# Kernel tuning notes

Measured on AMD Instinct MI355X. Metric: run time of the kernel, lower is better.

## Reference

```python
import jax, jax.numpy as jnp
import numpy as np

EMBED_DIM = 1024
NUM_HEADS = 16
HEAD_DIM = EMBED_DIM // NUM_HEADS
RANK = 512
B, S = 4, 4096


def setup_inputs() -> dict:
    key = jax.random.key(0)
    ks = jax.random.split(key, 16)
    sd = 0.02
    inp = {
        "query": jax.random.normal(ks[0], (B, S, EMBED_DIM), jnp.float32),
        "key": jax.random.normal(ks[1], (B, S, EMBED_DIM), jnp.float32),
        "value": jax.random.normal(ks[2], (B, S, EMBED_DIM), jnp.float32),
        # torch nn.Linear weights: [out_features, in_features]
        "q_down_w": jax.random.normal(ks[3], (RANK, EMBED_DIM), jnp.float32) * sd,
        "q_up_w": jax.random.normal(ks[4], (EMBED_DIM, RANK), jnp.float32) * sd,
        "q_up_b": jax.random.normal(ks[5], (EMBED_DIM,), jnp.float32) * sd,
        "k_down_w": jax.random.normal(ks[6], (RANK, EMBED_DIM), jnp.float32) * sd,
        "k_up_w": jax.random.normal(ks[7], (EMBED_DIM, RANK), jnp.float32) * sd,
        "k_up_b": jax.random.normal(ks[8], (EMBED_DIM,), jnp.float32) * sd,
        "v_down_w": jax.random.normal(ks[9], (RANK, EMBED_DIM), jnp.float32) * sd,
        "v_up_w": jax.random.normal(ks[10], (EMBED_DIM, RANK), jnp.float32) * sd,
        "v_up_b": jax.random.normal(ks[11], (EMBED_DIM,), jnp.float32) * sd,
        "out_w": jax.random.normal(ks[12], (EMBED_DIM, EMBED_DIM), jnp.float32) * sd,
        "out_b": jax.random.normal(ks[13], (EMBED_DIM,), jnp.float32) * sd,
    }
    return inp


def _linear(x, w, b=None):
    y = x @ w.T
    return y if b is None else y + b


def reference(query, key, value,
              q_down_w, q_up_w, q_up_b,
              k_down_w, k_up_w, k_up_b,
              v_down_w, v_up_w, v_up_b,
              out_w, out_b):
    b, s, _ = query.shape
    # low-rank QKV projections
    q = _linear(_linear(query, q_down_w), q_up_w, q_up_b)
    k = _linear(_linear(key, k_down_w), k_up_w, k_up_b)
    v = _linear(_linear(value, v_down_w), v_up_w, v_up_b)
    # [B,S,E] -> [B,H,S,Dh]
    q = q.reshape(b, s, NUM_HEADS, HEAD_DIM).transpose(0, 2, 1, 3)
    k = k.reshape(b, s, NUM_HEADS, HEAD_DIM).transpose(0, 2, 1, 3)
    v = v.reshape(b, s, NUM_HEADS, HEAD_DIM).transpose(0, 2, 1, 3)
    # kernel feature map: elu + 1  (note: scaling_factor in original is computed but unused)
    q = jax.nn.elu(q) + 1.0
    k = jax.nn.elu(k) + 1.0
    k_sum = k.sum(axis=-2)                              # [B,H,Dh]
    denom = jnp.einsum('bhnd,bhd->bhn', q, k_sum)       # [B,H,S]
    kv = jnp.einsum('bhnd,bhne->bhde', k, v)            # [B,H,Dh,Dh]
    num = jnp.einsum('bhnd,bhde->bhne', q, kv)          # [B,H,S,Dh]
    out = num / (denom[..., None] + 1e-6)
    out = out.transpose(0, 2, 1, 3).reshape(b, s, EMBED_DIM)
    return _linear(out, out_w, out_b)
```

## Files before the change

### kernel.cpp

```cpp
#include <hip/hip_runtime.h>
#include <hip/hip_bf16.h>

typedef unsigned short ushort_t;
typedef unsigned int uint_t;
typedef __attribute__((ext_vector_type(8))) short short8;
typedef __attribute__((ext_vector_type(4))) float f32x4;
typedef __attribute__((ext_vector_type(2))) float f32x2;

#define EMBED 1024
#define RANK  512
#define BB    4
#define SS    4096
#define HH    16
#define DHD   64
#define MM    (BB*SS)
#define NCHUNK 16

__device__ __forceinline__ float bf2f(ushort_t u) {
    union { uint_t i; float f; } v; v.i = ((uint_t)u) << 16; return v.f;
}
__device__ __forceinline__ float asf(uint_t u) {
    union { uint_t i; float f; } v; v.i = u; return v.f;
}
__device__ __forceinline__ ushort_t f2bf(float f) {
    union { float f; uint_t i; } v; v.f = f;
    uint_t r = v.i + 0x7FFFu + ((v.i >> 16) & 1u);
    return (ushort_t)(r >> 16);
}
__device__ __forceinline__ void gl2lds16(const void* g, void* l) {
    __builtin_amdgcn_global_load_lds((const __attribute__((address_space(1))) void*)g,
                                     (__attribute__((address_space(3))) void*)l,
                                     16, 0, 0);
}

template<int EPI>
__global__ __launch_bounds__(256) void gemm_bt(
    const ushort_t* __restrict__ A0, const ushort_t* __restrict__ A1, const ushort_t* __restrict__ A2,
    const ushort_t* __restrict__ B0, const ushort_t* __restrict__ B1, const ushort_t* __restrict__ B2,
    const float* __restrict__ bias0, const float* __restrict__ bias1, const float* __restrict__ bias2,
    void* __restrict__ C0, void* __restrict__ C1, void* __restrict__ C2,
    int N, int K, int nbx)
{
    __shared__ __align__(16) char lds_raw[49152];

    const int z = blockIdx.z;
    const ushort_t* Ab   = (z == 0) ? A0 : (z == 1) ? A1 : A2;
    const ushort_t* Bm   = (z == 0) ? B0 : (z == 1) ? B1 : B2;
    const float*    bias = (z == 0) ? bias0 : (z == 1) ? bias1 : bias2;
    void*           Cv   = (z == 0) ? C0 : (z == 1) ? C1 : C2;

    const int cpx = gridDim.x >> 3;
    const int bid = blockIdx.x;
    const int wg  = (bid & 7) * cpx + (bid >> 3);
    const long m0 = (long)(wg / nbx) * 128;
    const long n0 = (long)(wg % nbx) * 128;

    const int t = threadIdx.x;
    const int lane = t & 63;
    const int w = t >> 6;
    const int wr = (w >> 1) * 64;
    const int wc = (w & 1) * 64;
    const int fr = lane & 15;
    const int kq = (lane >> 4) * 8;

    const int srow = t >> 2;
    const int scol = ((t & 3) ^ ((srow >> 1) & 3)) * 8;
    const int kqs = (((kq >> 3) ^ ((fr >> 1) & 3))) * 8;

    auto STAGE = [&](int k0, int buf) {
        char* Ad = lds_raw + buf * 8192;
        char* Bd = lds_raw + 24576 + buf * 8192;
        #pragma unroll
        for (int ro = 0; ro < 2; ++ro) {
            const int row = ro * 64 + srow;
            gl2lds16(Ab + (m0 + row) * (long)K + k0 + scol, Ad + (ro * 256 + w * 64) * 16);
            gl2lds16(Bm + (n0 + row) * (long)K + k0 + scol, Bd + (ro * 256 + w * 64) * 16);
        }
    };

    f32x4 acc[4][4] = {};
    const int nt = K >> 5;

    STAGE(0, 0);
    STAGE(32, 1);

    int cur = 0;
    for (int ti = 0; ti < nt; ++ti) {
        if (ti + 1 < nt) { asm volatile("s_waitcnt vmcnt(4)" ::: "memory"); }
        else             { asm volatile("s_waitcnt vmcnt(0)" ::: "memory"); }
        __builtin_amdgcn_sched_barrier(0);
        __builtin_amdgcn_s_barrier();
        __builtin_amdgcn_sched_barrier(0);

        int nb = cur + 2; if (nb >= 3) nb -= 3;
        if (ti + 2 < nt) STAGE((ti + 2) << 5, nb);

        const ushort_t* Asc = (const ushort_t*)(lds_raw + cur * 8192);
        const ushort_t* Bsc = (const ushort_t*)(lds_raw + 24576 + cur * 8192);
        short8 av[4], bv[4];
        #pragma unroll
        for (int mi = 0; mi < 4; ++mi)
            av[mi] = *(const short8*)&Asc[(wr + mi * 16 + fr) * 32 + kqs];
        #pragma unroll
        for (int nf = 0; nf < 4; ++nf)
            bv[nf] = *(const short8*)&Bsc[(wc + nf * 16 + fr) * 32 + kqs];
        #pragma unroll
        for (int mi = 0; mi < 4; ++mi)
            #pragma unroll
            for (int nf = 0; nf < 4; ++nf)
                acc[mi][nf] = __builtin_amdgcn_mfma_f32_16x16x32_bf16(
                    av[mi], bv[nf], acc[mi][nf], 0, 0, 0);

        ++cur; if (cur == 3) cur = 0;
    }

    const int rj = (lane >> 4) * 4;
    if (EPI == 3) {
        float* Cf = (float*)Cv;
        __syncthreads();
        #pragma unroll
        for (int nf = 0; nf < 4; ++nf) {
            const long col = n0 + wc + nf * 16 + fr;
            const float bval = bias[col];
            #pragma unroll
            for (int mi = 0; mi < 4; ++mi)
                #pragma unroll
                for (int j = 0; j < 4; ++j)
                    Cf[(m0 + wr + mi * 16 + rj + j) * (long)N + col] = acc[mi][nf][j] + bval;
        }
    } else {
        ushort_t* Ct = (ushort_t*)lds_raw;
        __syncthreads();
        const bool do_elu = (EPI == 2) && (z < 2);
        #pragma unroll
        for (int nf = 0; nf < 4; ++nf) {
            const int coll = wc + nf * 16 + fr;
            const float bval = (EPI >= 2) ? bias[n0 + coll] : 0.0f;
            #pragma unroll
            for (int mi = 0; mi < 4; ++mi) {
                #pragma unroll
                for (int j = 0; j < 4; ++j) {
                    float x = acc[mi][nf][j];
                    if (EPI >= 2) x += bval;
                    if (do_elu) x = (x > 0.0f) ? (x + 1.0f) : __expf(x);
                    Ct[(wr + mi * 16 + rj + j) * 136 + coll] = f2bf(x);
                }
            }
        }
        __syncthreads();
        ushort_t* Cb = (ushort_t*)Cv;
        #pragma unroll
        for (int it = 0; it < 8; ++it) {
            const int idx = it * 256 + t;
            const int r   = idx >> 4;
            const int c8  = (idx & 15) * 8;
            short8 vv = *(const short8*)&Ct[r * 136 + c8];
            *(short8*)(Cb + (m0 + r) * (long)N + n0 + c8) = vv;
        }
    }
}

__global__ __launch_bounds__(256) void cvt_act(const float* __restrict__ q,
                                               const float* __restrict__ k,
                                               const float* __restrict__ v,
                                               ushort_t* __restrict__ qo,
                                               ushort_t* __restrict__ ko,
                                               ushort_t* __restrict__ vo)
{
    const long NTOT   = (long)3 * MM * EMBED;
    const long stride = (long)2048 * 256 * 8;
    long i = ((long)blockIdx.x * 256 + threadIdx.x) * 8;
    for (; i < NTOT; i += stride) {
        const int  zz  = (int)(i >> 24);
        const long off = i & 0xFFFFFF;
        const float* src = (zz == 0) ? q : (zz == 1) ? k : v;
        ushort_t*    dst = (zz == 0) ? qo : (zz == 1) ? ko : vo;
        f32x4 f0 = *(const f32x4*)(src + off);
        f32x4 f1 = *(const f32x4*)(src + off + 4);
        short8 h;
        h[0] = (short)f2bf(f0[0]); h[1] = (short)f2bf(f0[1]);
        h[2] = (short)f2bf(f0[2]); h[3] = (short)f2bf(f0[3]);
        h[4] = (short)f2bf(f1[0]); h[5] = (short)f2bf(f1[1]);
        h[6] = (short)f2bf(f1[2]); h[7] = (short)f2bf(f1[3]);
        *(short8*)(dst + off) = h;
    }
}

__global__ __launch_bounds__(256) void cvt_weights(
    const float* __restrict__ s0, const float* __restrict__ s1,
    const float* __restrict__ s2, const float* __restrict__ s3,
    const float* __restrict__ s4, const float* __restrict__ s5,
    const float* __restrict__ s6,
    ushort_t* __restrict__ d0, ushort_t* __restrict__ d1,
    ushort_t* __restrict__ d2, ushort_t* __restrict__ d3,
    ushort_t* __restrict__ d4, ushort_t* __restrict__ d5,
    ushort_t* __restrict__ d6)
{
    const int y = blockIdx.y;
    const float* src; ushort_t* dst; int n;
    switch (y) {
        case 0: src = s0; dst = d0; n = RANK * EMBED; break;
        case 1: src = s1; dst = d1; n = RANK * EMBED; break;
        case 2: src = s2; dst = d2; n = RANK * EMBED; break;
        case 3: src = s3; dst = d3; n = RANK * EMBED; break;
        case 4: src = s4; dst = d4; n = RANK * EMBED; break;
        case 5: src = s5; dst = d5; n = RANK * EMBED; break;
        default: src = s6; dst = d6; n = EMBED * EMBED; break;
    }
    const int i = (blockIdx.x * 256 + threadIdx.x) * 4;
    if (i < n) {
        f32x4 f = *(const f32x4*)(src + i);
        typedef __attribute__((ext_vector_type(4))) short short4v;
        short4v h;
        h[0] = (short)f2bf(f[0]); h[1] = (short)f2bf(f[1]);
        h[2] = (short)f2bf(f[2]); h[3] = (short)f2bf(f[3]);
        *(short4v*)(dst + i) = h;
    }
}

__global__ __launch_bounds__(256) void kv_stats(const ushort_t* __restrict__ Kp,
                                                const ushort_t* __restrict__ Vp,
                                                float* __restrict__ kvp,
                                                float* __restrict__ ksump)
{
    __shared__ __align__(16) ushort_t Ks[64 * 64];
    __shared__ __align__(16) ushort_t Vs[64 * 64];
    const int t = threadIdx.x;
    const int w = t >> 6;
    const int bh = blockIdx.x;
    const int chunk = blockIdx.y;
    const int b = bh >> 4, h = bh & 15;
    const int d0 = (t & 15) * 4;
    const int e0 = (t >> 4) * 4;
    f32x2 acc2[4][2] = {};
    f32x2 sks2[2] = {};
    const long hbase = ((long)b * SS) * EMBED + h * DHD;

    for (int sub = 0; sub < 4; ++sub) {
        const int n00 = chunk * 256 + sub * 64;
        #pragma unroll
        for (int ro = 0; ro < 2; ++ro) {
            const int idx = ro * 256 + t;
            const int r = idx >> 3, c16 = idx & 7;
            const long g = hbase + (long)(n00 + r) * EMBED + c16 * 8;
            gl2lds16(Kp + g, (char*)Ks + (ro * 256 + w * 64) * 16);
            gl2lds16(Vp + g, (char*)Vs + (ro * 256 + w * 64) * 16);
        }
        __syncthreads();
        #pragma unroll 8
        for (int n = 0; n < 64; ++n) {
            const uint_t* kr = (const uint_t*)(Ks + n * 64 + d0);
            const uint_t* vr = (const uint_t*)(Vs + n * 64 + e0);
            const uint_t k01 = kr[0], k23 = kr[1];
            const uint_t v01 = vr[0], v23 = vr[1];
            f32x2 kd0, kd1;
            kd0[0] = asf(k01 << 16); kd0[1] = asf(k01 & 0xffff0000u);
            kd1[0] = asf(k23 << 16); kd1[1] = asf(k23 & 0xffff0000u);
            float ve[4];
            ve[0] = asf(v01 << 16); ve[1] = asf(v01 & 0xffff0000u);
            ve[2] = asf(v23 << 16); ve[3] = asf(v23 & 0xffff0000u);
            #pragma unroll
            for (int e = 0; e < 4; ++e) {
                f32x2 vb; vb[0] = ve[e]; vb[1] = ve[e];
                acc2[e][0] += vb * kd0;
                acc2[e][1] += vb * kd1;
            }
            if (e0 == 0) { sks2[0] += kd0; sks2[1] += kd1; }
        }
        __syncthreads();
    }

    float* dst = kvp + ((long)chunk * 64 + bh) * 4096;
    #pragma unroll
    for (int e = 0; e < 4; ++e) {
        f32x4 vv;
        vv[0] = acc2[e][0][0]; vv[1] = acc2[e][0][1];
        vv[2] = acc2[e][1][0]; vv[3] = acc2[e][1][1];
        *(f32x4*)(dst + (e0 + e) * 64 + d0) = vv;
    }
    if (e0 == 0) {
        float* sd = ksump + ((long)chunk * 64 + bh) * 64 + d0;
        sd[0] = sks2[0][0]; sd[1] = sks2[0][1];
        sd[2] = sks2[1][0]; sd[3] = sks2[1][1];
    }
}

__global__ __launch_bounds__(256) void kv_reduce(const float* __restrict__ kvp,
                                                 const float* __restrict__ ksump,
                                                 ushort_t* __restrict__ kvb,
                                                 float* __restrict__ ksumf)
{
    const int bh = blockIdx.x;
    const int t = threadIdx.x;
    const long base = (long)bh * 4096 + t * 16;
    f32x4 s[4] = {};
    #pragma unroll 4
    for (int c = 0; c < NCHUNK; ++c) {
        const float* src = kvp + (long)c * 64 * 4096 + base;
        #pragma unroll
        for (int j = 0; j < 4; ++j) s[j] += *(const f32x4*)(src + j * 4);
    }
    short8 o0, o1;
    #pragma unroll
    for (int j = 0; j < 4; ++j) {
        o0[j]     = (short)f2bf(s[0][j]); o0[4 + j] = (short)f2bf(s[1][j]);
        o1[j]     = (short)f2bf(s[2][j]); o1[4 + j] = (short)f2bf(s[3][j]);
    }
    *(short8*)(kvb + base)     = o0;
    *(short8*)(kvb + base + 8) = o1;

    if (t < 64) {
        float ss = 0.f;
        #pragma unroll
        for (int c = 0; c < NCHUNK; ++c) ss += ksump[(long)c * 64 * 64 + bh * 64 + t];
        ksumf[bh * 64 + t] = ss;
    }
}

__global__ __launch_bounds__(256) void attn_out(const ushort_t* __restrict__ Qp,
                                                const ushort_t* __restrict__ kvb,
                                                const float* __restrict__ ksum,
                                                ushort_t* __restrict__ Op)
{
    __shared__ __align__(16) ushort_t Qs[128 * 64];
    __shared__ __align__(16) ushort_t KVs[64 * 64];
    __shared__ float kss[64];
    __shared__ float dnm[128];
    const int t = threadIdx.x;
    const int w = t >> 6, lane = t & 63;
    const int bh = blockIdx.x, mc = blockIdx.y;
    const int b = bh >> 4, h = bh & 15;
    const long base = ((long)b * SS + mc * 128) * EMBED + h * DHD;

    #pragma unroll
    for (int ro = 0; ro < 4; ++ro) {
        const int idx = ro * 256 + t;
        const int r = idx >> 3, c16 = idx & 7;
        gl2lds16(Qp + base + (long)r * EMBED + c16 * 8,
                 (char*)Qs + (ro * 256 + w * 64) * 16);
    }
    #pragma unroll
    for (int ro = 0; ro < 2; ++ro) {
        const int idx = ro * 256 + t;
        gl2lds16(kvb + (long)bh * 4096 + idx * 8,
                 (char*)KVs + (ro * 256 + w * 64) * 16);
    }
    if (t < 64) kss[t] = ksum[bh * 64 + t];
    __syncthreads();

    if (t < 128) {
        float s = 0.f;
        const uint_t* qr = (const uint_t*)(Qs + t * 64);
        #pragma unroll
        for (int jj = 0; jj < 32; ++jj) {
            const uint_t u = qr[jj];
            union { uint_t i; float f; } lo, hi;
            lo.i = u << 16; hi.i = u & 0xffff0000u;
            s += lo.f * kss[2 * jj] + hi.f * kss[2 * jj + 1];
        }
        dnm[t] = s;
    }

    const int fr = lane & 15, kq = (lane >> 4) * 8;
    f32x4 acc[2][4] = {};
    #pragma unroll
    for (int ks = 0; ks < 2; ++ks) {
        short8 av[2], bv[4];
        #pragma unroll
        for (int mi = 0; mi < 2; ++mi)
            av[mi] = *(const short8*)&Qs[(w * 32 + mi * 16 + fr) * 64 + ks * 32 + kq];
        #pragma unroll
        for (int nf = 0; nf < 4; ++nf)
            bv[nf] = *(const short8*)&KVs[(nf * 16 + fr) * 64 + ks * 32 + kq];
        #pragma unroll
        for (int mi = 0; mi < 2; ++mi)
            #pragma unroll
            for (int nf = 0; nf < 4; ++nf)
                acc[mi][nf] = __builtin_amdgcn_mfma_f32_16x16x32_bf16(
                    av[mi], bv[nf], acc[mi][nf], 0, 0, 0);
    }
    __syncthreads();

    const int rj = (lane >> 4) * 4;
    #pragma unroll
    for (int mi = 0; mi < 2; ++mi) {
        #pragma unroll
        for (int nf = 0; nf < 4; ++nf) {
            #pragma unroll
            for (int j = 0; j < 4; ++j) {
                const int r = w * 32 + mi * 16 + rj + j;
                const int c = nf * 16 + fr;
                const float x = acc[mi][nf][j] / (dnm[r] + 1e-6f);
                Op[base + (long)r * EMBED + c] = f2bf(x);
            }
        }
    }
}

extern "C" void kernel_launch(void* const* d_in, const int* in_sizes, int n_in,
                              void* d_out, int out_size, void* d_ws, size_t ws_size,
                              hipStream_t stream)
{
    (void)in_sizes; (void)n_in; (void)out_size; (void)ws_size;
    const float* query = (const float*)d_in[0];
    const float* key_  = (const float*)d_in[1];
    const float* value = (const float*)d_in[2];
    const float* q_dw  = (const float*)d_in[3];
    const float* q_uw  = (const float*)d_in[4];
    const float* q_ub  = (const float*)d_in[5];
    const float* k_dw  = (const float*)d_in[6];
    const float* k_uw  = (const float*)d_in[7];
    const float* k_ub  = (const float*)d_in[8];
    const float* v_dw  = (const float*)d_in[9];
    const float* v_uw  = (const float*)d_in[10];
    const float* v_ub  = (const float*)d_in[11];
    const float* o_w   = (const float*)d_in[12];
    const float* o_b   = (const float*)d_in[13];

    char* ws = (char*)d_ws;
    size_t off = 0;
    auto alloc = [&](size_t bytes) -> void* {
        void* p = ws + off;
        off += (bytes + 255) & ~(size_t)255;
        return p;
    };
    const size_t WSMALL = (size_t)RANK * EMBED;
    ushort_t* bw_qd = (ushort_t*)alloc(WSMALL * 2);
    ushort_t* bw_qu = (ushort_t*)alloc(WSMALL * 2);
    ushort_t* bw_kd = (ushort_t*)alloc(WSMALL * 2);
    ushort_t* bw_ku = (ushort_t*)alloc(WSMALL * 2);
    ushort_t* bw_vd = (ushort_t*)alloc(WSMALL * 2);
    ushort_t* bw_vu = (ushort_t*)alloc(WSMALL * 2);
    ushort_t* bw_o  = (ushort_t*)alloc((size_t)EMBED * EMBED * 2);
    ushort_t* Qb    = (ushort_t*)alloc((size_t)MM * EMBED * 2);
    ushort_t* Kb    = (ushort_t*)alloc((size_t)MM * EMBED * 2);
    ushort_t* Vb    = (ushort_t*)alloc((size_t)MM * EMBED * 2);
    ushort_t* Y1q   = (ushort_t*)alloc((size_t)MM * RANK * 2);
    ushort_t* Y1k   = (ushort_t*)alloc((size_t)MM * RANK * 2);
    ushort_t* Y1v   = (ushort_t*)alloc((size_t)MM * RANK * 2);
    float*    ksump = (float*)alloc((size_t)NCHUNK * 64 * 64 * 4);
    float*    ksumf = (float*)alloc((size_t)64 * 64 * 4);
    ushort_t* kvb   = (ushort_t*)alloc((size_t)64 * 64 * 64 * 2);

    ushort_t* PQ = Qb;
    ushort_t* PK = Kb;
    ushort_t* PV = Vb;
    float*    kvp = (float*)Y1q;
    ushort_t* O   = Y1k;

    const dim3 blk(256);

    cvt_act<<<dim3(2048), blk, 0, stream>>>(query, key_, value, Qb, Kb, Vb);
    cvt_weights<<<dim3(EMBED * EMBED / 1024, 7), blk, 0, stream>>>(
        q_dw, q_uw, k_dw, k_uw, v_dw, v_uw, o_w,
        bw_qd, bw_qu, bw_kd, bw_ku, bw_vd, bw_vu, bw_o);

    gemm_bt<0><<<dim3(MM / 128 * (RANK / 128), 1, 3), blk, 0, stream>>>(
        Qb, Kb, Vb,
        bw_qd, bw_kd, bw_vd,
        nullptr, nullptr, nullptr,
        Y1q, Y1k, Y1v,
        RANK, EMBED, RANK / 128);

    gemm_bt<2><<<dim3(MM / 128 * (EMBED / 128), 1, 3), blk, 0, stream>>>(
        Y1q, Y1k, Y1v,
        bw_qu, bw_ku, bw_vu,
        q_ub, k_ub, v_ub,
        PQ, PK, PV,
        EMBED, RANK, EMBED / 128);

    kv_stats<<<dim3(64, NCHUNK), blk, 0, stream>>>(PK, PV, kvp, ksump);
    kv_reduce<<<dim3(64), blk, 0, stream>>>(kvp, ksump, kvb, ksumf);
    attn_out<<<dim3(64, 32), blk, 0, stream>>>(PQ, kvb, ksumf, O);

    gemm_bt<3><<<dim3(MM / 128 * (EMBED / 128), 1, 1), blk, 0, stream>>>(
        O, nullptr, nullptr,
        bw_o, nullptr, nullptr,
        o_b, nullptr, nullptr,
        d_out, nullptr, nullptr,
        EMBED, EMBED, EMBED / 128);
}
```

Before: 302.3 us.

## Enlarge GEMM tiles to 256x256 with 512 threads and BK=64 double buffering

Reworks the shared bf16 GEMM kernel from 128x128 tiles with 4 waves to 256x256 tiles with 8 waves. The K step grows to 64 and the pipeline becomes a two-buffer LDS scheme with a new XOR swizzle. The goal is more operand reuse per LDS byte and fewer global loads per flop. The epilogue staging is also re-swizzled for the wider tile. In exchange it uses 128KB of LDS and 128 accumulator registers per lane, so each CU holds only one block. The launch grid also shrinks a lot, for example to 256 blocks for the output projection, which risks poor load balance and wave quantization.

New measurement: 316.4 us. 1.05x slower.

```diff
diff --git a/kernel.cpp b/kernel.cpp
--- a/kernel.cpp
+++ b/kernel.cpp
@@ -34,14 +34,14 @@
 }
 
 template<int EPI>
-__global__ __launch_bounds__(256) void gemm_bt(
+__global__ __launch_bounds__(512, 2) void gemm_bt(
     const ushort_t* __restrict__ A0, const ushort_t* __restrict__ A1, const ushort_t* __restrict__ A2,
     const ushort_t* __restrict__ B0, const ushort_t* __restrict__ B1, const ushort_t* __restrict__ B2,
     const float* __restrict__ bias0, const float* __restrict__ bias1, const float* __restrict__ bias2,
     void* __restrict__ C0, void* __restrict__ C1, void* __restrict__ C2,
     int N, int K, int nbx)
 {
-    __shared__ __align__(16) char lds_raw[49152];
+    __shared__ __align__(16) char lds_raw[131072];
 
     const int z = blockIdx.z;
     const ushort_t* Ab   = (z == 0) ? A0 : (z == 1) ? A1 : A2;
@@ -52,69 +52,88 @@
     const int cpx = gridDim.x >> 3;
     const int bid = blockIdx.x;
     const int wg  = (bid & 7) * cpx + (bid >> 3);
-    const long m0 = (long)(wg / nbx) * 128;
-    const long n0 = (long)(wg % nbx) * 128;
-
-    const int t = threadIdx.x;
+    const long m0 = (long)(wg / nbx) * 256;
+    const long n0 = (long)(wg % nbx) * 256;
+
+    const int t    = threadIdx.x;
     const int lane = t & 63;
-    const int w = t >> 6;
-    const int wr = (w >> 1) * 64;
-    const int wc = (w & 1) * 64;
-    const int fr = lane & 15;
-    const int kq = (lane >> 4) * 8;
-
-    const int srow = t >> 2;
-    const int scol = ((t & 3) ^ ((srow >> 1) & 3)) * 8;
-    const int kqs = (((kq >> 3) ^ ((fr >> 1) & 3))) * 8;
-
-    auto STAGE = [&](int k0, int buf) {
-        char* Ad = lds_raw + buf * 8192;
-        char* Bd = lds_raw + 24576 + buf * 8192;
-        #pragma unroll
-        for (int ro = 0; ro < 2; ++ro) {
-            const int row = ro * 64 + srow;
-            gl2lds16(Ab + (m0 + row) * (long)K + k0 + scol, Ad + (ro * 256 + w * 64) * 16);
-            gl2lds16(Bm + (n0 + row) * (long)K + k0 + scol, Bd + (ro * 256 + w * 64) * 16);
-        }
+    const int w    = t >> 6;
+    const int wr   = (w >> 2) * 128;
+    const int wc   = (w & 3) * 64;
+    const int fr   = lane & 15;
+    const int kq4  = lane >> 4;
+    const int fx   = fr & 7;
+
+    const int srow = t >> 3;
+    const int scol = ((t & 7) ^ (srow & 7)) * 8;
+    const int sdst = w * 1024;
+
+    const int Abase = (w >> 2) * 16384;
+    const int Bbase = 32768 + ((w >> 1) & 1) * 16384;
+    const int nsub  = (w & 1) * 64;
+
+    auto STAGE_ALL = [&](int k0, int buf) {
+        const int bb = buf * 65536;
+        #pragma unroll
+        for (int h = 0; h < 2; ++h)
+            #pragma unroll
+            for (int ro = 0; ro < 2; ++ro)
+                gl2lds16(Ab + (m0 + h * 128 + ro * 64 + srow) * (long)K + k0 + scol,
+                         lds_raw + bb + h * 16384 + ro * 8192 + sdst);
+        #pragma unroll
+        for (int h = 0; h < 2; ++h)
+            #pragma unroll
+            for (int ro = 0; ro < 2; ++ro)
+                gl2lds16(Bm + (n0 + h * 128 + ro * 64 + srow) * (long)K + k0 + scol,
+                         lds_raw + bb + 32768 + h * 16384 + ro * 8192 + sdst);
     };
 
-    f32x4 acc[4][4] = {};
-    const int nt = K >> 5;
-
-    STAGE(0, 0);
-    STAGE(32, 1);
+    f32x4 acc[8][4] = {};
+    const int nt = K >> 6;
+
+    STAGE_ALL(0, 0);
 
     int cur = 0;
     for (int ti = 0; ti < nt; ++ti) {
-        if (ti + 1 < nt) { asm volatile("s_waitcnt vmcnt(4)" ::: "memory"); }
-        else             { asm volatile("s_waitcnt vmcnt(0)" ::: "memory"); }
+        if (ti + 1 < nt) {
+            STAGE_ALL((ti + 1) << 6, cur ^ 1);
+            asm volatile("s_waitcnt vmcnt(8)" ::: "memory");
+        } else {
+            asm volatile("s_waitcnt vmcnt(0)" ::: "memory");
+        }
         __builtin_amdgcn_sched_barrier(0);
         __builtin_amdgcn_s_barrier();
         __builtin_amdgcn_sched_barrier(0);
 
-        int nb = cur + 2; if (nb >= 3) nb -= 3;
-        if (ti + 2 < nt) STAGE((ti + 2) << 5, nb);
-
-        const ushort_t* Asc = (const ushort_t*)(lds_raw + cur * 8192);
-        const ushort_t* Bsc = (const ushort_t*)(lds_raw + 24576 + cur * 8192);
-        short8 av[4], bv[4];
-        #pragma unroll
-        for (int mi = 0; mi < 4; ++mi)
-            av[mi] = *(const short8*)&Asc[(wr + mi * 16 + fr) * 32 + kqs];
-        #pragma unroll
-        for (int nf = 0; nf < 4; ++nf)
-            bv[nf] = *(const short8*)&Bsc[(wc + nf * 16 + fr) * 32 + kqs];
-        #pragma unroll
-        for (int mi = 0; mi < 4; ++mi)
+        const ushort_t* As_ = (const ushort_t*)(lds_raw + cur * 65536 + Abase);
+        const ushort_t* Bs_ = (const ushort_t*)(lds_raw + cur * 65536 + Bbase);
+        #pragma unroll
+        for (int kk = 0; kk < 2; ++kk) {
+            const int sl = ((kk * 4 + kq4) ^ fx) * 8;
+            short8 bv[4];
             #pragma unroll
             for (int nf = 0; nf < 4; ++nf)
-                acc[mi][nf] = __builtin_amdgcn_mfma_f32_16x16x32_bf16(
-                    av[mi], bv[nf], acc[mi][nf], 0, 0, 0);
-
-        ++cur; if (cur == 3) cur = 0;
-    }
-
-    const int rj = (lane >> 4) * 4;
+                bv[nf] = *(const short8*)&Bs_[(nsub + nf * 16 + fr) * 64 + sl];
+            #pragma unroll
+            for (int mh = 0; mh < 2; ++mh) {
+                short8 av[4];
+                #pragma unroll
+                for (int mi = 0; mi < 4; ++mi)
+                    av[mi] = *(const short8*)&As_[(mh * 64 + mi * 16 + fr) * 64 + sl];
+                #pragma unroll
+                for (int mi = 0; mi < 4; ++mi)
+                    #pragma unroll
+                    for (int nf = 0; nf < 4; ++nf)
+                        acc[mh * 4 + mi][nf] = __builtin_amdgcn_mfma_f32_16x16x32_bf16(
+                            av[mi], bv[nf], acc[mh * 4 + mi][nf], 0, 0, 0);
+            }
+        }
+        __builtin_amdgcn_sched_barrier(0);
+        __builtin_amdgcn_s_barrier();
+        cur ^= 1;
+    }
+
+    const int rj = kq4 * 4;
     if (EPI == 3) {
         float* Cf = (float*)Cv;
         __syncthreads();
@@ -123,39 +142,40 @@
             const long col = n0 + wc + nf * 16 + fr;
             const float bval = bias[col];
             #pragma unroll
-            for (int mi = 0; mi < 4; ++mi)
+            for (int mg = 0; mg < 8; ++mg)
                 #pragma unroll
                 for (int j = 0; j < 4; ++j)
-                    Cf[(m0 + wr + mi * 16 + rj + j) * (long)N + col] = acc[mi][nf][j] + bval;
+                    Cf[(m0 + wr + mg * 16 + rj + j) * (long)N + col] = acc[mg][nf][j] + bval;
         }
     } else {
+        __syncthreads();
         ushort_t* Ct = (ushort_t*)lds_raw;
-        __syncthreads();
         const bool do_elu = (EPI == 2) && (z < 2);
         #pragma unroll
         for (int nf = 0; nf < 4; ++nf) {
-            const int coll = wc + nf * 16 + fr;
-            const float bval = (EPI >= 2) ? bias[n0 + coll] : 0.0f;
-            #pragma unroll
-            for (int mi = 0; mi < 4; ++mi) {
+            const int c_loc = wc + nf * 16 + fr;
+            const float bval = (EPI >= 2) ? bias[n0 + c_loc] : 0.0f;
+            #pragma unroll
+            for (int mg = 0; mg < 8; ++mg) {
                 #pragma unroll
                 for (int j = 0; j < 4; ++j) {
-                    float x = acc[mi][nf][j];
+                    const int r_loc = wr + mg * 16 + rj + j;
+                    float x = acc[mg][nf][j];
                     if (EPI >= 2) x += bval;
                     if (do_elu) x = (x > 0.0f) ? (x + 1.0f) : __expf(x);
-                    Ct[(wr + mi * 16 + rj + j) * 136 + coll] = f2bf(x);
+                    Ct[r_loc * 256 + (((c_loc >> 3) ^ (r_loc & 7)) * 8) + (c_loc & 7)] = f2bf(x);
                 }
             }
         }
         __syncthreads();
         ushort_t* Cb = (ushort_t*)Cv;
         #pragma unroll
-        for (int it = 0; it < 8; ++it) {
-            const int idx = it * 256 + t;
-            const int r   = idx >> 4;
-            const int c8  = (idx & 15) * 8;
-            short8 vv = *(const short8*)&Ct[r * 136 + c8];
-            *(short8*)(Cb + (m0 + r) * (long)N + n0 + c8) = vv;
+        for (int it = 0; it < 16; ++it) {
+            const int idx = it * 512 + t;
+            const int r   = idx >> 5;
+            const int s16 = idx & 31;
+            short8 vv = *(const short8*)&Ct[r * 256 + ((s16 ^ (r & 7)) * 8)];
+            *(short8*)(Cb + (m0 + r) * (long)N + n0 + s16 * 8) = vv;
         }
     }
 }
@@ -449,34 +469,35 @@
     ushort_t* O   = Y1k;
 
     const dim3 blk(256);
+    const dim3 blk2(512);
 
     cvt_act<<<dim3(2048), blk, 0, stream>>>(query, key_, value, Qb, Kb, Vb);
     cvt_weights<<<dim3(EMBED * EMBED / 1024, 7), blk, 0, stream>>>(
         q_dw, q_uw, k_dw, k_uw, v_dw, v_uw, o_w,
         bw_qd, bw_qu, bw_kd, bw_ku, bw_vd, bw_vu, bw_o);
 
-    gemm_bt<0><<<dim3(MM / 128 * (RANK / 128), 1, 3), blk, 0, stream>>>(
+    gemm_bt<0><<<dim3(MM / 256 * (RANK / 256), 1, 3), blk2, 0, stream>>>(
         Qb, Kb, Vb,
         bw_qd, bw_kd, bw_vd,
         nullptr, nullptr, nullptr,
         Y1q, Y1k, Y1v,
-        RANK, EMBED, RANK / 128);
-
-    gemm_bt<2><<<dim3(MM / 128 * (EMBED / 128), 1, 3), blk, 0, stream>>>(
+        RANK, EMBED, RANK / 256);
+
+    gemm_bt<2><<<dim3(MM / 256 * (EMBED / 256), 1, 3), blk2, 0, stream>>>(
         Y1q, Y1k, Y1v,
         bw_qu, bw_ku, bw_vu,
         q_ub, k_ub, v_ub,
         PQ, PK, PV,
-        EMBED, RANK, EMBED / 128);
+        EMBED, RANK, EMBED / 256);
 
     kv_stats<<<dim3(64, NCHUNK), blk, 0, stream>>>(PK, PV, kvp, ksump);
     kv_reduce<<<dim3(64), blk, 0, stream>>>(kvp, ksump, kvb, ksumf);
     attn_out<<<dim3(64, 32), blk, 0, stream>>>(PQ, kvb, ksumf, O);
 
-    gemm_bt<3><<<dim3(MM / 128 * (EMBED / 128), 1, 1), blk, 0, stream>>>(
+    gemm_bt<3><<<dim3(MM / 256 * (EMBED / 256), 1, 1), blk2, 0, stream>>>(
         O, nullptr, nullptr,
         bw_o, nullptr, nullptr,
         o_b, nullptr, nullptr,
         d_out, nullptr, nullptr,
-        EMBED, EMBED, EMBED / 128);
-}
+        EMBED, EMBED, EMBED / 256);
+}
```
